# Performance work log

Measured on AMD Instinct MI355X. Metric: run time of the kernel, lower is better.

Reference implementation:

```python
import jax, jax.numpy as jnp
import numpy as np
from jax import lax

B_, DIM, H, W, Dd = 2, 256, 16, 16, 16
DI, N, DTR, K = 256, 8, 16, 4   # d_inner (expand=1), d_state, dt_rank=ceil(256/16), d_conv
OUT_C = 1200
L = H * W * Dd
EPS = 1e-5


def setup_inputs() -> dict:
    key = jax.random.key(0)
    ks = jax.random.split(key, 20)
    g = lambda k, s: jax.random.normal(k, s, jnp.float32) * 0.02
    A_log = jnp.log(jnp.broadcast_to(jnp.arange(1, N + 1, dtype=jnp.float32), (DI, N)))
    dt_bias = jnp.full((DI,), float(np.log(np.expm1(0.01))), jnp.float32)
    return {
        "input0": jax.random.normal(ks[0], (B_, DIM, H, W, Dd), jnp.float32),
        "input1": jax.random.normal(ks[1], (B_, DIM, H, W, Dd), jnp.float32),
        "norm0_w": jnp.ones((DIM,), jnp.float32),
        "norm0_b": jnp.zeros((DIM,), jnp.float32),
        "norm1_w": jnp.ones((DIM,), jnp.float32),
        "norm1_b": jnp.zeros((DIM,), jnp.float32),
        "in_proj_w": g(ks[2], (DI, DIM)),
        "in_projz_w": g(ks[3], (DI, DIM)),
        "conv1d_w": g(ks[4], (DI, 1, K)),
        "conv1d_bias": jnp.zeros((DI,), jnp.float32),
        "conv1db_w": g(ks[5], (DI, 1, K)),
        "conv1db_bias": jnp.zeros((DI,), jnp.float32),
        "xproj_w": g(ks[6], (DTR + 2 * N, DI)),
        "xprojb_w": g(ks[7], (DTR + 2 * N, DI)),
        "dtproj_w": g(ks[8], (DI, DTR)),
        "dtproj_bias": dt_bias,
        "dtprojb_w": g(ks[9], (DI, DTR)),
        "dtprojb_bias": dt_bias,
        "A_log": A_log,
        "Ab_log": A_log,
        "D_p": jnp.ones((DI,), jnp.float32),
        "D_b": jnp.ones((DI,), jnp.float32),
        "rms_w": jnp.ones((DI,), jnp.float32),
        "out_proj_w": g(ks[10], (DIM, DI)),
        "conv3d_w": g(ks[11], (OUT_C, DIM)),
        "conv3d_bias": jnp.zeros((OUT_C,), jnp.float32),
    }


def _layernorm(x, w, b):
    m = x.mean(-1, keepdims=True)
    v = ((x - m) ** 2).mean(-1, keepdims=True)
    return (x - m) * lax.rsqrt(v + EPS) * w + b


def _rmsnorm(x, w):
    return x * lax.rsqrt((x * x).mean(-1, keepdims=True) + EPS) * w


def _ssm_dir(x, z, conv_w, conv_b, xproj_w, dtproj_w, dtproj_bias, A_log, Dp):
    # One direction of the bimamba-v2 selective scan. x, z: (b, L, d_inner)
    xt = x.transpose(0, 2, 1)  # (b, d, L)
    xc = lax.conv_general_dilated(xt, conv_w, (1,), [(K - 1, 0)], feature_group_count=DI)
    x = jax.nn.silu(xc + conv_b[None, :, None]).transpose(0, 2, 1)  # causal dw-conv + silu
    dbl = x @ xproj_w.T                                   # (b, L, dt_rank + 2n)
    dt, Bm, Cm = dbl[..., :DTR], dbl[..., DTR:DTR + N], dbl[..., DTR + N:]
    dt = jax.nn.softplus(dt @ dtproj_w.T + dtproj_bias)    # (b, L, d)
    A = -jnp.exp(A_log)                                    # (d, n)
    dA = jnp.exp(dt[..., None] * A)                        # (b, L, d, n)
    dBu = (dt * x)[..., None] * Bm[:, :, None, :]          # (b, L, d, n)

    def step(h, inp):
        dA_t, dBu_t, C_t = inp
        h = h * dA_t + dBu_t
        return h, jnp.einsum('bdn,bn->bd', h, C_t)

    h0 = jnp.zeros((x.shape[0], DI, N), x.dtype)
    _, ys = lax.scan(step, h0, (dA.transpose(1, 0, 2, 3), dBu.transpose(1, 0, 2, 3), Cm.transpose(1, 0, 2)))
    y = ys.transpose(1, 0, 2) + x * Dp                     # (b, L, d)
    return y * jax.nn.silu(z)                              # gate from the matching branch


def _forward(input0, input1, norm0_w, norm0_b, norm1_w, norm1_b, in_proj_w, in_projz_w,
             conv1d_w, conv1d_bias, conv1db_w, conv1db_bias, xproj_w, xprojb_w,
             dtproj_w, dtproj_bias, dtprojb_w, dtprojb_bias, A_log, Ab_log,
             D_p, D_b, rms_w, out_proj_w, conv3d_w, conv3d_bias):
    b = input0.shape[0]
    skip = input0
    seq0 = input0.transpose(0, 2, 3, 4, 1).reshape(b, L, DIM)  # b (h w d) c
    seq1 = input1.transpose(0, 2, 3, 4, 1).reshape(b, L, DIM)
    seq0 = _layernorm(seq0, norm0_w, norm0_b)
    seq1 = _layernorm(seq1, norm1_w, norm1_b)
    x = seq0 @ in_proj_w.T    # SSM input from input0
    z = seq1 @ in_projz_w.T   # gate from extra_emb (input1)
    y_f = _ssm_dir(x, z, conv1d_w, conv1d_bias, xproj_w, dtproj_w, dtproj_bias, A_log, D_p)
    y_b = _ssm_dir(x[:, ::-1], z[:, ::-1], conv1db_w, conv1db_bias, xprojb_w,
                   dtprojb_w, dtprojb_bias, Ab_log, D_b)[:, ::-1]

    def head(y):
        o = _rmsnorm(y, rms_w) @ out_proj_w.T              # use_norm=True, then out_proj
        o = o.reshape(b, H, W, Dd, DIM).transpose(0, 4, 1, 2, 3) + skip
        return jnp.einsum('bchwd,oc->bohwd', o, conv3d_w) + conv3d_bias[None, :, None, None, None]

    out = head((y_f + y_b) * 0.5)   # if_devide_out=True
    return out, head(y_f), head(y_b)


def reference(input0, input1, norm0_w, norm0_b, norm1_w, norm1_b, in_proj_w, in_projz_w,
              conv1d_w, conv1d_bias, conv1db_w, conv1db_bias, xproj_w, xprojb_w,
              dtproj_w, dtproj_bias, dtprojb_w, dtprojb_bias, A_log, Ab_log,
              D_p, D_b, rms_w, out_proj_w, conv3d_w, conv3d_bias):
    return _forward(input0, input1, norm0_w, norm0_b, norm1_w, norm1_b, in_proj_w, in_projz_w,
                    conv1d_w, conv1d_bias, conv1db_w, conv1db_bias, xproj_w, xprojb_w,
                    dtproj_w, dtproj_bias, dtprojb_w, dtprojb_bias, A_log, Ab_log,
                    D_p, D_b, rms_w, out_proj_w, conv3d_w, conv3d_bias)
```

## Files before the change

### kernel.cpp

```cpp
#include <hip/hip_runtime.h>
#include <cstdint>

#define NTOK 8192

typedef __attribute__((ext_vector_type(4))) float f32x4;
typedef __attribute__((ext_vector_type(8))) short s16x8;

__device__ __forceinline__ short f2bf(float f) {
  union { float f; unsigned u; } x; x.f = f;
  unsigned r = x.u + 0x7FFFu + ((x.u >> 16) & 1u);
  return (short)(r >> 16);
}
__device__ __forceinline__ float bf2f(short s) {
  union { float f; unsigned u; } x;
  x.u = ((unsigned)(unsigned short)s) << 16;
  return x.f;
}
__device__ __forceinline__ void gl_lds16(const void* g, void* l) {
  __builtin_amdgcn_global_load_lds((const unsigned int*)g, (unsigned int*)l, 16, 0, 0);
}

__global__ __launch_bounds__(256) void ln_transpose_kernel(
    const float* __restrict__ in0, const float* __restrict__ in1,
    const float* __restrict__ w0, const float* __restrict__ b0,
    const float* __restrict__ w1, const float* __restrict__ b1,
    const float* __restrict__ wxp, const float* __restrict__ wzp,
    const float* __restrict__ wop, const float* __restrict__ wcp,
    short* __restrict__ Wx, short* __restrict__ Wz,
    short* __restrict__ Wo, short* __restrict__ Wc,
    short* __restrict__ xlnz, float* __restrict__ seqT)
{
  __shared__ float tile[32 * 257];
  __shared__ float mu[32], rs[32];
  const int tid = threadIdx.x;
  const int b  = blockIdx.x >> 7;
  const int l0 = (blockIdx.x & 127) << 5;

  {
    int base = (int)blockIdx.x << 11;
    #pragma unroll
    for (int i = 0; i < 8; ++i) {
      int idx = base + (i << 8) + tid;
      if (idx < 65536)       Wx[idx] = f2bf(wxp[idx]);
      else if (idx < 131072) Wz[idx - 65536] = f2bf(wzp[idx - 65536]);
      else if (idx < 196608) Wo[idx - 131072] = f2bf(wop[idx - 131072]);
      else {
        int k = idx - 196608;
        Wc[k] = ((k >> 8) < 1200) ? f2bf(wcp[k]) : (short)0;
      }
    }
  }

  for (int pass = 0; pass < 2; ++pass) {
    const float* in = pass ? in1 : in0;
    #pragma unroll 8
    for (int i = 0; i < 32; ++i) {
      int e = (i << 8) + tid;
      int c = e >> 5, lo = e & 31;
      tile[lo * 257 + c] = in[((size_t)(b * 256 + c) << 12) + l0 + lo];
    }
    __syncthreads();
    if (tid < 64) {
      int r = tid & 31, h = tid >> 5;
      float s = 0.f, ss = 0.f;
      #pragma unroll 16
      for (int c = h * 128; c < h * 128 + 128; ++c) {
        float v = tile[r * 257 + c];
        s += v; ss += v * v;
      }
      s  += __shfl_xor(s, 32, 64);
      ss += __shfl_xor(ss, 32, 64);
      if (h == 0) {
        float m = s * (1.f / 256.f);
        mu[r] = m;
        rs[r] = rsqrtf(ss * (1.f / 256.f) - m * m + 1e-5f);
      }
    }
    __syncthreads();
    const float* w  = pass ? w1 : w0;
    const float* bb = pass ? b1 : b0;
    float wv = w[tid], bv = bb[tid];
    #pragma unroll 8
    for (int i = 0; i < 32; ++i) {
      float v = tile[i * 257 + tid];
      int row = (pass ? 8192 : 0) + (b << 12) + l0 + i;
      xlnz[(size_t)row * 256 + tid] = f2bf((v - mu[i]) * rs[i] * wv + bv);
      if (pass == 0) seqT[(((size_t)b << 12) + l0 + i) * 256 + tid] = v;
    }
    __syncthreads();
  }
}

template <int EPI>
__global__ __launch_bounds__(256) void gemm_fast(
    const short* __restrict__ A, const short* __restrict__ W0,
    const short* __restrict__ W1, float* __restrict__ Cf,
    short* __restrict__ Cb, const float* __restrict__ ADD,
    const float* __restrict__ bias, int Msplit)
{
  __shared__ short As[4096];
  __shared__ short Bs[4096];
  const int tid  = threadIdx.x;
  const int lane = tid & 63, wave = tid >> 6;
  const int m0 = blockIdx.y << 7;
  const int n0 = blockIdx.x << 7;
  const short* W = (EPI == 0 && m0 >= Msplit) ? W1 : W0;

  const int sr = tid >> 2;
  const int sc = (tid & 3) << 3;
  const int mf = lane & 15, kq = lane >> 4;
  const int wm = (wave & 1) << 6, wn = (wave >> 1) << 6;

  const short* Ar0 = A + (size_t)(m0 + sr) * 256 + sc;
  const short* Ar1 = A + (size_t)(m0 + 64 + sr) * 256 + sc;
  const short* Br0 = W + (size_t)(n0 + sr) * 256 + sc;
  const short* Br1 = W + (size_t)(n0 + 64 + sr) * 256 + sc;
  short* AsW = &As[wave << 9];
  short* BsW = &Bs[wave << 9];

  f32x4 acc[4][4] = {};

  for (int kt = 0; kt < 256; kt += 32) {
    gl_lds16(Ar0 + kt, AsW);
    gl_lds16(Ar1 + kt, AsW + 2048);
    gl_lds16(Br0 + kt, BsW);
    gl_lds16(Br1 + kt, BsW + 2048);
    __syncthreads();
    s16x8 af[4], bfr[4];
    #pragma unroll
    for (int i = 0; i < 4; ++i)
      af[i] = *(const s16x8*)&As[((wm + (i << 4) + mf) << 5) + (kq << 3)];
    #pragma unroll
    for (int j = 0; j < 4; ++j)
      bfr[j] = *(const s16x8*)&Bs[((wn + (j << 4) + mf) << 5) + (kq << 3)];
    #pragma unroll
    for (int i = 0; i < 4; ++i)
      #pragma unroll
      for (int j = 0; j < 4; ++j)
        acc[i][j] = __builtin_amdgcn_mfma_f32_16x16x32_bf16(af[i], bfr[j], acc[i][j], 0, 0, 0);
    __syncthreads();
  }

  if (EPI == 0) {
    #pragma unroll
    for (int i = 0; i < 4; ++i) {
      int gm = m0 + wm + (i << 4) + (kq << 2);
      #pragma unroll
      for (int j = 0; j < 4; ++j) {
        int gn = n0 + wn + (j << 4) + mf;
        #pragma unroll
        for (int r = 0; r < 4; ++r)
          Cf[(size_t)(gm + r) * 256 + gn] = acc[i][j][r];
      }
    }
  } else if (EPI == 1) {
    #pragma unroll
    for (int i = 0; i < 4; ++i) {
      int gm = m0 + wm + (i << 4) + (kq << 2);
      #pragma unroll
      for (int j = 0; j < 4; ++j) {
        int gn = n0 + wn + (j << 4) + mf;
        #pragma unroll
        for (int r = 0; r < 4; ++r) {
          int tok = (gm + r) & 8191;
          float v = acc[i][j][r] + ADD[(size_t)tok * 256 + gn];
          Cb[(size_t)(gm + r) * 256 + gn] = f2bf(v);
        }
      }
    }
  } else {
    const int head = m0 >> 13, bb = (m0 >> 12) & 1, lb = m0 & 4095;
    float* obase = Cf + (size_t)head * (2u * 1200u * 4096u) + (size_t)bb * (1200u * 4096u);
    #pragma unroll
    for (int i = 0; i < 4; ++i) {
      int l = lb + wm + (i << 4) + (kq << 2);
      #pragma unroll
      for (int j = 0; j < 4; ++j) {
        int gn = n0 + wn + (j << 4) + mf;
        if (gn < 1200) {
          float bv = bias[gn];
          f32x4 v = acc[i][j];
          v[0] += bv; v[1] += bv; v[2] += bv; v[3] += bv;
          __builtin_nontemporal_store(v, (f32x4*)&obase[(size_t)gn * 4096 + l]);
        }
      }
    }
  }
}

__global__ __launch_bounds__(256) void fused_front(
    const float* __restrict__ x,
    const float* __restrict__ cw0, const float* __restrict__ cb0,
    const float* __restrict__ cw1, const float* __restrict__ cb1,
    const float* __restrict__ xw0, const float* __restrict__ xw1,
    const float* __restrict__ dtw0, const float* __restrict__ dtb0,
    const float* __restrict__ dtw1, const float* __restrict__ dtb1,
    const float* __restrict__ Alog0, const float* __restrict__ Alog1,
    float* __restrict__ xcg, float* __restrict__ dblg,
    float* __restrict__ P, float* __restrict__ Q)
{
  __shared__ float xcs[16 * 256];
  __shared__ short wxs[256 * 33];
  __shared__ float dls[512];
  const int tid = threadIdx.x;
  const int dir = blockIdx.x >> 9;
  const int b   = (blockIdx.x >> 8) & 1;
  const int ch  = blockIdx.x & 255;
  const int t0  = ch << 4;
  const float* cw   = dir ? cw1 : cw0;
  const float* cb   = dir ? cb1 : cb0;
  const float* xw   = dir ? xw1 : xw0;
  const float* dtw  = dir ? dtw1 : dtw0;
  const float* dtb  = dir ? dtb1 : dtb0;
  const float* Alog = dir ? Alog1 : Alog0;
  const size_t dS = (size_t)dir * (NTOK * 256);
  const size_t xb = ((size_t)b) << 12;

  {
    const int d = tid;
    const float w0 = cw[(d << 2)], w1 = cw[(d << 2) + 1],
                w2 = cw[(d << 2) + 2], w3 = cw[(d << 2) + 3];
    const float bias = cb[d];
    float h0 = 0.f, h1 = 0.f, h2 = 0.f;
    #pragma unroll
    for (int i = 0; i < 3; ++i) {
      int ts = t0 - 3 + i; float v = 0.f;
      if (ts >= 0) { int tn = dir ? 4095 - ts : ts; v = x[(xb + tn) * 256 + d]; }
      h0 = h1; h1 = h2; h2 = v;
    }
    #pragma unroll
    for (int s = 0; s < 16; ++s) {
      int ts = t0 + s;
      int tn = dir ? 4095 - ts : ts;
      float xv = x[(xb + tn) * 256 + d];
      float a = bias + w0 * h0 + w1 * h1 + w2 * h2 + w3 * xv;
      h0 = h1; h1 = h2; h2 = xv;
      float v = a / (1.f + __expf(-a));
      xcs[s * 256 + d] = v;
      xcg[dS + (xb + ts) * 256 + d] = v;
    }
  }
  #pragma unroll
  for (int i = 0; i < 32; ++i) {
    int flat = (i << 8) + tid;
    wxs[(flat & 255) * 33 + (flat >> 8)] = f2bf(xw[flat]);
  }
  __syncthreads();

  {
    const int j = tid & 31, s0 = tid >> 5;
    float a0 = 0.f, a1 = 0.f;
    #pragma unroll 8
    for (int r = 0; r < 256; ++r) {
      float w = bf2f(wxs[r * 33 + j]);
      a0 = fmaf(xcs[s0 * 256 + r], w, a0);
      a1 = fmaf(xcs[(s0 + 8) * 256 + r], w, a1);
    }
    dls[(s0 << 5) + j] = a0;
    dls[((s0 + 8) << 5) + j] = a1;
    size_t db = (size_t)dir * 262144 + ((xb + t0) << 5);
    dblg[db + tid] = a0;
    dblg[db + 256 + tid] = a1;
  }
  __syncthreads();

  {
    const int d = tid;
    float wrow[16];
    #pragma unroll
    for (int r = 0; r < 16; ++r) wrow[r] = dtw[(d << 4) + r];
    const float bias = dtb[d];
    float Av[8], p[8], q[8];
    #pragma unroll
    for (int n = 0; n < 8; ++n) {
      Av[n] = -expf(Alog[(d << 3) + n]); p[n] = 1.f; q[n] = 0.f;
    }
    for (int s = 0; s < 16; ++s) {
      float a = bias;
      #pragma unroll
      for (int r = 0; r < 16; ++r) a = fmaf(dls[(s << 5) + r], wrow[r], a);
      float dtv = (a > 20.f) ? a : log1pf(__expf(a));
      float xv = xcs[s * 256 + d];
      float du = dtv * xv;
      #pragma unroll
      for (int n = 0; n < 8; ++n) {
        float dA = __expf(dtv * Av[n]);
        p[n] *= dA;
        q[n] = fmaf(q[n], dA, du * dls[(s << 5) + 16 + n]);
      }
    }
    size_t ob = (size_t)dir * 1048576 + ((size_t)((b << 8) + ch) * 8) * 256 + d;
    #pragma unroll
    for (int n = 0; n < 8; ++n) { P[ob + (n << 8)] = p[n]; Q[ob + (n << 8)] = q[n]; }
  }
}

__global__ __launch_bounds__(256) void scan_p2(
    const float* __restrict__ P, const float* __restrict__ Q, float* __restrict__ Hs)
{
  const int d = threadIdx.x;
  const int bid = blockIdx.x;
  const int dir = bid >> 4, b = (bid >> 3) & 1, n = bid & 7;
  const size_t dOff = (size_t)dir * 1048576;
  float h = 0.f;
  #pragma unroll 8
  for (int ch = 0; ch < 256; ++ch) {
    size_t i = dOff + ((size_t)((b << 8) + ch) * 8 + n) * 256 + d;
    Hs[i] = h;
    h = fmaf(P[i], h, Q[i]);
  }
}

__global__ __launch_bounds__(256) void scan_p3(
    const float* __restrict__ xcg, const float* __restrict__ dblg,
    const float* __restrict__ dtw0, const float* __restrict__ dtb0,
    const float* __restrict__ dtw1, const float* __restrict__ dtb1,
    const float* __restrict__ Hs, const float* __restrict__ z,
    const float* __restrict__ Alog0, const float* __restrict__ Alog1,
    const float* __restrict__ Dp0, const float* __restrict__ Dp1,
    short* __restrict__ yall)
{
  __shared__ float dl[512];
  const int d = threadIdx.x;
  const int dir = blockIdx.x >> 9;
  const int b   = (blockIdx.x >> 8) & 1;
  const int ch  = blockIdx.x & 255;
  const int t0  = ch << 4;
  const float* dtw  = dir ? dtw1 : dtw0;
  const float* dtb  = dir ? dtb1 : dtb0;
  const float* Alog = dir ? Alog1 : Alog0;
  const float* Dp   = dir ? Dp1 : Dp0;
  const size_t dS = (size_t)dir * (NTOK * 256);
  const size_t xb = ((size_t)b) << 12;
  short* y = yall + (size_t)dir * (NTOK * 256);

  size_t db = (size_t)dir * 262144 + ((xb + t0) << 5);
  dl[d]       = dblg[db + d];
  dl[256 + d] = dblg[db + 256 + d];
  float wrow[16];
  #pragma unroll
  for (int r = 0; r < 16; ++r) wrow[r] = dtw[(d << 4) + r];
  const float bias = dtb[d];
  float Av[8], h[8];
  #pragma unroll
  for (int n = 0; n < 8; ++n) Av[n] = -expf(Alog[(d << 3) + n]);
  size_t hb = (size_t)dir * 1048576 + ((size_t)((b << 8) + ch) * 8) * 256 + d;
  #pragma unroll
  for (int n = 0; n < 8; ++n) h[n] = Hs[hb + (n << 8)];
  const float Dv = Dp[d];
  __syncthreads();
  for (int s = 0; s < 16; ++s) {
    float a = bias;
    #pragma unroll
    for (int r = 0; r < 16; ++r) a = fmaf(dl[(s << 5) + r], wrow[r], a);
    float dtv = (a > 20.f) ? a : log1pf(__expf(a));
    int ts = t0 + s;
    float xv = xcg[dS + (xb + ts) * 256 + d];
    float du = dtv * xv;
    float yv = 0.f;
    #pragma unroll
    for (int n = 0; n < 8; ++n) {
      float dA = __expf(dtv * Av[n]);
      h[n] = fmaf(h[n], dA, du * dl[(s << 5) + 16 + n]);
      yv = fmaf(h[n], dl[(s << 5) + 24 + n], yv);
    }
    yv = fmaf(xv, Dv, yv);
    int tn = dir ? (4095 - ts) : ts;
    size_t zi = (xb + tn) * 256 + d;
    float zv = z[zi];
    y[zi] = f2bf(yv * zv / (1.f + __expf(-zv)));
  }
}

__global__ __launch_bounds__(256) void rms_all(
    const short* __restrict__ yf, const short* __restrict__ yb,
    const float* __restrict__ w, short* __restrict__ yn)
{
  const int d = threadIdx.x;
  const int mode = blockIdx.y;
  const size_t tok = blockIdx.x;
  size_t i = tok * 256 + d;
  float v;
  if (mode == 0)      v = 0.5f * (bf2f(yf[i]) + bf2f(yb[i]));
  else if (mode == 1) v = bf2f(yf[i]);
  else                v = bf2f(yb[i]);
  float ss = v * v;
  #pragma unroll
  for (int o = 32; o > 0; o >>= 1) ss += __shfl_xor(ss, o, 64);
  __shared__ float red[4];
  if ((d & 63) == 0) red[d >> 6] = ss;
  __syncthreads();
  float tot = red[0] + red[1] + red[2] + red[3];
  float sc = rsqrtf(tot * (1.f / 256.f) + 1e-5f);
  yn[((size_t)mode * 8192 + tok) * 256 + d] = f2bf(v * sc * w[d]);
}

extern "C" void kernel_launch(void* const* d_in, const int* in_sizes, int n_in,
                              void* d_out, int out_size, void* d_ws, size_t ws_size,
                              hipStream_t stream) {
  const float* in0        = (const float*)d_in[0];
  const float* in1        = (const float*)d_in[1];
  const float* n0w        = (const float*)d_in[2];
  const float* n0b        = (const float*)d_in[3];
  const float* n1w        = (const float*)d_in[4];
  const float* n1b        = (const float*)d_in[5];
  const float* in_proj_w  = (const float*)d_in[6];
  const float* in_projz_w = (const float*)d_in[7];
  const float* conv1d_w   = (const float*)d_in[8];
  const float* conv1d_b   = (const float*)d_in[9];
  const float* conv1db_w  = (const float*)d_in[10];
  const float* conv1db_b  = (const float*)d_in[11];
  const float* xproj_w    = (const float*)d_in[12];
  const float* xprojb_w   = (const float*)d_in[13];
  const float* dtproj_w   = (const float*)d_in[14];
  const float* dtproj_b   = (const float*)d_in[15];
  const float* dtprojb_w  = (const float*)d_in[16];
  const float* dtprojb_b  = (const float*)d_in[17];
  const float* A_log      = (const float*)d_in[18];
  const float* Ab_log     = (const float*)d_in[19];
  const float* D_p        = (const float*)d_in[20];
  const float* D_b        = (const float*)d_in[21];
  const float* rms_w      = (const float*)d_in[22];
  const float* out_proj_w = (const float*)d_in[23];
  const float* conv3d_w   = (const float*)d_in[24];
  const float* conv3d_b   = (const float*)d_in[25];
  (void)in_sizes; (void)n_in; (void)out_size; (void)ws_size;

  float* ws = (float*)d_ws;
  size_t o = 0;
  short* xlnz = (short*)(ws + o); o += 2097152;
  float* seqT = ws + o;           o += 2097152;
  float* x    = ws + o;           o += 2097152;
  float* z    = ws + o;           o += 2097152;
  float* xc2  = ws + o;           o += 4194304;
  float* dbl2 = ws + o;           o += 524288;
  float* P    = ws + o;           o += 2097152;
  float* Q    = ws + o;           o += 2097152;
  float* Hs   = ws + o;           o += 2097152;
  short* yall = (short*)(ws + o); o += 2097152;
  short* yn   = (short*)(ws + o); o += 3145728;
  short* obuf = (short*)(ws + o); o += 3145728;
  short* Wx   = (short*)(ws + o); o += 32768;
  short* Wz   = (short*)(ws + o); o += 32768;
  short* Wo   = (short*)(ws + o); o += 32768;
  short* Wc   = (short*)(ws + o); o += 163840;
  float* out  = (float*)d_out;

  dim3 blk(256);

  ln_transpose_kernel<<<dim3(256), blk, 0, stream>>>(
      in0, in1, n0w, n0b, n1w, n1b,
      in_proj_w, in_projz_w, out_proj_w, conv3d_w, Wx, Wz, Wo, Wc,
      xlnz, seqT);

  gemm_fast<0><<<dim3(2, 128), blk, 0, stream>>>(xlnz, Wx, Wz, x, nullptr, nullptr, nullptr, 8192);

  fused_front<<<dim3(1024), blk, 0, stream>>>(
      x, conv1d_w, conv1d_b, conv1db_w, conv1db_b,
      xproj_w, xprojb_w, dtproj_w, dtproj_b, dtprojb_w, dtprojb_b,
      A_log, Ab_log, xc2, dbl2, P, Q);

  scan_p2<<<dim3(32), blk, 0, stream>>>(P, Q, Hs);

  scan_p3<<<dim3(1024), blk, 0, stream>>>(
      xc2, dbl2, dtproj_w, dtproj_b, dtprojb_w, dtprojb_b,
      Hs, z, A_log, Ab_log, D_p, D_b, yall);

  rms_all<<<dim3(8192, 3), blk, 0, stream>>>(yall, yall + 2097152, rms_w, yn);
  gemm_fast<1><<<dim3(2, 192), blk, 0, stream>>>(yn, Wo, nullptr, nullptr, obuf, seqT, nullptr, 0);
  gemm_fast<2><<<dim3(10, 192), blk, 0, stream>>>(obuf, Wc, nullptr, out, nullptr, nullptr, conv3d_b, 0);
}
```

Baseline: 338.7 us.

## Split LN passes across blocks, double-buffer GEMM, widen scan_p2, vectorize rmsnorm

The layernorm/transpose kernel now gives each block a single input tensor, so the grid doubles and the serial two-pass loop goes away. The bf16 GEMM gets double-buffered LDS, so the next K-tile's global-to-LDS load is issued before the MFMAs on the current tile. The sequential chunk-carry scan now runs 64-thread blocks across 128 blocks instead of 32 blocks, giving more CUs work on this latency-bound step. RMSnorm handles one token per wave with 4-wide vector loads and stores and no cross-wave LDS reduction. These changes cost extra LDS per GEMM block and add complexity across several kernels.

```diff
diff --git a/kernel.cpp b/kernel.cpp
--- a/kernel.cpp
+++ b/kernel.cpp
@@ -5,6 +5,7 @@
 
 typedef __attribute__((ext_vector_type(4))) float f32x4;
 typedef __attribute__((ext_vector_type(8))) short s16x8;
+typedef __attribute__((ext_vector_type(4))) short s16x4;
 
 __device__ __forceinline__ short f2bf(float f) {
   union { float f; unsigned u; } x; x.f = f;
@@ -32,14 +33,15 @@
 {
   __shared__ float tile[32 * 257];
   __shared__ float mu[32], rs[32];
-  const int tid = threadIdx.x;
-  const int b  = blockIdx.x >> 7;
-  const int l0 = (blockIdx.x & 127) << 5;
+  const int tid  = threadIdx.x;
+  const int pass = blockIdx.x >> 8;
+  const int b    = (blockIdx.x >> 7) & 1;
+  const int l0   = (blockIdx.x & 127) << 5;
 
   {
-    int base = (int)blockIdx.x << 11;
-    #pragma unroll
-    for (int i = 0; i < 8; ++i) {
+    int base = (int)blockIdx.x << 10;
+    #pragma unroll
+    for (int i = 0; i < 4; ++i) {
       int idx = base + (i << 8) + tid;
       if (idx < 65536)       Wx[idx] = f2bf(wxp[idx]);
       else if (idx < 131072) Wz[idx - 65536] = f2bf(wzp[idx - 65536]);
@@ -51,43 +53,40 @@
     }
   }
 
-  for (int pass = 0; pass < 2; ++pass) {
-    const float* in = pass ? in1 : in0;
-    #pragma unroll 8
-    for (int i = 0; i < 32; ++i) {
-      int e = (i << 8) + tid;
-      int c = e >> 5, lo = e & 31;
-      tile[lo * 257 + c] = in[((size_t)(b * 256 + c) << 12) + l0 + lo];
-    }
-    __syncthreads();
-    if (tid < 64) {
-      int r = tid & 31, h = tid >> 5;
-      float s = 0.f, ss = 0.f;
-      #pragma unroll 16
-      for (int c = h * 128; c < h * 128 + 128; ++c) {
-        float v = tile[r * 257 + c];
-        s += v; ss += v * v;
-      }
-      s  += __shfl_xor(s, 32, 64);
-      ss += __shfl_xor(ss, 32, 64);
-      if (h == 0) {
-        float m = s * (1.f / 256.f);
-        mu[r] = m;
-        rs[r] = rsqrtf(ss * (1.f / 256.f) - m * m + 1e-5f);
-      }
-    }
-    __syncthreads();
-    const float* w  = pass ? w1 : w0;
-    const float* bb = pass ? b1 : b0;
-    float wv = w[tid], bv = bb[tid];
-    #pragma unroll 8
-    for (int i = 0; i < 32; ++i) {
-      float v = tile[i * 257 + tid];
-      int row = (pass ? 8192 : 0) + (b << 12) + l0 + i;
-      xlnz[(size_t)row * 256 + tid] = f2bf((v - mu[i]) * rs[i] * wv + bv);
-      if (pass == 0) seqT[(((size_t)b << 12) + l0 + i) * 256 + tid] = v;
-    }
-    __syncthreads();
+  const float* in = pass ? in1 : in0;
+  #pragma unroll 8
+  for (int i = 0; i < 32; ++i) {
+    int e = (i << 8) + tid;
+    int c = e >> 5, lo = e & 31;
+    tile[lo * 257 + c] = in[((size_t)(b * 256 + c) << 12) + l0 + lo];
+  }
+  __syncthreads();
+  if (tid < 64) {
+    int r = tid & 31, hh = tid >> 5;
+    float s = 0.f, ss = 0.f;
+    #pragma unroll 16
+    for (int c = hh * 128; c < hh * 128 + 128; ++c) {
+      float v = tile[r * 257 + c];
+      s += v; ss += v * v;
+    }
+    s  += __shfl_xor(s, 32, 64);
+    ss += __shfl_xor(ss, 32, 64);
+    if (hh == 0) {
+      float m = s * (1.f / 256.f);
+      mu[r] = m;
+      rs[r] = rsqrtf(ss * (1.f / 256.f) - m * m + 1e-5f);
+    }
+  }
+  __syncthreads();
+  const float* w  = pass ? w1 : w0;
+  const float* bb = pass ? b1 : b0;
+  float wv = w[tid], bv = bb[tid];
+  #pragma unroll 8
+  for (int i = 0; i < 32; ++i) {
+    float v = tile[i * 257 + tid];
+    int row = (pass ? 8192 : 0) + (b << 12) + l0 + i;
+    xlnz[(size_t)row * 256 + tid] = f2bf((v - mu[i]) * rs[i] * wv + bv);
+    if (pass == 0) seqT[(((size_t)b << 12) + l0 + i) * 256 + tid] = v;
   }
 }
 
@@ -98,8 +97,8 @@
     short* __restrict__ Cb, const float* __restrict__ ADD,
     const float* __restrict__ bias, int Msplit)
 {
-  __shared__ short As[4096];
-  __shared__ short Bs[4096];
+  __shared__ short As[2][4096];
+  __shared__ short Bs[2][4096];
   const int tid  = threadIdx.x;
   const int lane = tid & 63, wave = tid >> 6;
   const int m0 = blockIdx.y << 7;
@@ -115,24 +114,33 @@
   const short* Ar1 = A + (size_t)(m0 + 64 + sr) * 256 + sc;
   const short* Br0 = W + (size_t)(n0 + sr) * 256 + sc;
   const short* Br1 = W + (size_t)(n0 + 64 + sr) * 256 + sc;
-  short* AsW = &As[wave << 9];
-  short* BsW = &Bs[wave << 9];
+  const int wo = wave << 9;
 
   f32x4 acc[4][4] = {};
 
-  for (int kt = 0; kt < 256; kt += 32) {
-    gl_lds16(Ar0 + kt, AsW);
-    gl_lds16(Ar1 + kt, AsW + 2048);
-    gl_lds16(Br0 + kt, BsW);
-    gl_lds16(Br1 + kt, BsW + 2048);
-    __syncthreads();
+  gl_lds16(Ar0, &As[0][wo]);
+  gl_lds16(Ar1, &As[0][wo + 2048]);
+  gl_lds16(Br0, &Bs[0][wo]);
+  gl_lds16(Br1, &Bs[0][wo + 2048]);
+  __syncthreads();
+
+  #pragma unroll
+  for (int t = 0; t < 8; ++t) {
+    const int cur = t & 1;
+    if (t < 7) {
+      const int kt = (t + 1) << 5;
+      gl_lds16(Ar0 + kt, &As[cur ^ 1][wo]);
+      gl_lds16(Ar1 + kt, &As[cur ^ 1][wo + 2048]);
+      gl_lds16(Br0 + kt, &Bs[cur ^ 1][wo]);
+      gl_lds16(Br1 + kt, &Bs[cur ^ 1][wo + 2048]);
+    }
     s16x8 af[4], bfr[4];
     #pragma unroll
     for (int i = 0; i < 4; ++i)
-      af[i] = *(const s16x8*)&As[((wm + (i << 4) + mf) << 5) + (kq << 3)];
+      af[i] = *(const s16x8*)&As[cur][((wm + (i << 4) + mf) << 5) + (kq << 3)];
     #pragma unroll
     for (int j = 0; j < 4; ++j)
-      bfr[j] = *(const s16x8*)&Bs[((wn + (j << 4) + mf) << 5) + (kq << 3)];
+      bfr[j] = *(const s16x8*)&Bs[cur][((wn + (j << 4) + mf) << 5) + (kq << 3)];
     #pragma unroll
     for (int i = 0; i < 4; ++i)
       #pragma unroll
@@ -295,11 +303,11 @@
   }
 }
 
-__global__ __launch_bounds__(256) void scan_p2(
+__global__ __launch_bounds__(64) void scan_p2(
     const float* __restrict__ P, const float* __restrict__ Q, float* __restrict__ Hs)
 {
-  const int d = threadIdx.x;
-  const int bid = blockIdx.x;
+  const int d   = ((blockIdx.x & 3) << 6) + threadIdx.x;
+  const int bid = blockIdx.x >> 2;
   const int dir = bid >> 4, b = (bid >> 3) & 1, n = bid & 7;
   const size_t dOff = (size_t)dir * 1048576;
   float h = 0.f;
@@ -376,23 +384,34 @@
     const short* __restrict__ yf, const short* __restrict__ yb,
     const float* __restrict__ w, short* __restrict__ yn)
 {
-  const int d = threadIdx.x;
+  const int lane = threadIdx.x & 63, wave = threadIdx.x >> 6;
   const int mode = blockIdx.y;
-  const size_t tok = blockIdx.x;
-  size_t i = tok * 256 + d;
-  float v;
-  if (mode == 0)      v = 0.5f * (bf2f(yf[i]) + bf2f(yb[i]));
-  else if (mode == 1) v = bf2f(yf[i]);
-  else                v = bf2f(yb[i]);
-  float ss = v * v;
+  const size_t tok = ((size_t)blockIdx.x << 2) + wave;
+  const size_t base = tok * 256 + (lane << 2);
+  float v0, v1, v2, v3;
+  if (mode == 0) {
+    s16x4 a = *(const s16x4*)&yf[base];
+    s16x4 c = *(const s16x4*)&yb[base];
+    v0 = 0.5f * (bf2f(a[0]) + bf2f(c[0]));
+    v1 = 0.5f * (bf2f(a[1]) + bf2f(c[1]));
+    v2 = 0.5f * (bf2f(a[2]) + bf2f(c[2]));
+    v3 = 0.5f * (bf2f(a[3]) + bf2f(c[3]));
+  } else {
+    const short* yy = (mode == 1) ? yf : yb;
+    s16x4 a = *(const s16x4*)&yy[base];
+    v0 = bf2f(a[0]); v1 = bf2f(a[1]); v2 = bf2f(a[2]); v3 = bf2f(a[3]);
+  }
+  float ss = v0 * v0 + v1 * v1 + v2 * v2 + v3 * v3;
   #pragma unroll
   for (int o = 32; o > 0; o >>= 1) ss += __shfl_xor(ss, o, 64);
-  __shared__ float red[4];
-  if ((d & 63) == 0) red[d >> 6] = ss;
-  __syncthreads();
-  float tot = red[0] + red[1] + red[2] + red[3];
-  float sc = rsqrtf(tot * (1.f / 256.f) + 1e-5f);
-  yn[((size_t)mode * 8192 + tok) * 256 + d] = f2bf(v * sc * w[d]);
+  float sc = rsqrtf(ss * (1.f / 256.f) + 1e-5f);
+  f32x4 wv = *(const f32x4*)&w[lane << 2];
+  s16x4 r;
+  r[0] = f2bf(v0 * sc * wv[0]);
+  r[1] = f2bf(v1 * sc * wv[1]);
+  r[2] = f2bf(v2 * sc * wv[2]);
+  r[3] = f2bf(v3 * sc * wv[3]);
+  *(s16x4*)&yn[((size_t)mode * 8192 + tok) * 256 + (lane << 2)] = r;
 }
 
 extern "C" void kernel_launch(void* const* d_in, const int* in_sizes, int n_in,
@@ -448,7 +467,7 @@
 
   dim3 blk(256);
 
-  ln_transpose_kernel<<<dim3(256), blk, 0, stream>>>(
+  ln_transpose_kernel<<<dim3(512), blk, 0, stream>>>(
       in0, in1, n0w, n0b, n1w, n1b,
       in_proj_w, in_projz_w, out_proj_w, conv3d_w, Wx, Wz, Wo, Wc,
       xlnz, seqT);
@@ -460,13 +479,13 @@
       xproj_w, xprojb_w, dtproj_w, dtproj_b, dtprojb_w, dtprojb_b,
       A_log, Ab_log, xc2, dbl2, P, Q);
 
-  scan_p2<<<dim3(32), blk, 0, stream>>>(P, Q, Hs);
+  scan_p2<<<dim3(128), dim3(64), 0, stream>>>(P, Q, Hs);
 
   scan_p3<<<dim3(1024), blk, 0, stream>>>(
       xc2, dbl2, dtproj_w, dtproj_b, dtprojb_w, dtprojb_b,
       Hs, z, A_log, Ab_log, D_p, D_b, yall);
 
-  rms_all<<<dim3(8192, 3), blk, 0, stream>>>(yall, yall + 2097152, rms_w, yn);
+  rms_all<<<dim3(2048, 3), blk, 0, stream>>>(yall, yall + 2097152, rms_w, yn);
   gemm_fast<1><<<dim3(2, 192), blk, 0, stream>>>(yn, Wo, nullptr, nullptr, obuf, seqT, nullptr, 0);
   gemm_fast<2><<<dim3(10, 192), blk, 0, stream>>>(obuf, Wc, nullptr, out, nullptr, nullptr, conv3d_b, 0);
 }
```

Result: no change. 342.9 us (+1.2%).
